# Kernel tuning notes

Hardware: AMD Instinct MI355X
Metric: run time of the kernel (lower is better)

## Reference

```python
import jax, jax.numpy as jnp
import numpy as np

H, W = 512, 512  # image_size from init_kwargs


def _render_single(xyz, color, opacity):
    """Faithful JAX version of GaussianRenderer._fallback_render (the path the
    module executes when the CUDA rasterizer is unavailable), vectorized.
    Point-splat each Gaussian to one pixel, depth-sort descending (back-to-front),
    alpha-composite: a_k = o_k * prod_{j<k}(1 - o_j); depth = z of front-most hit.
    xyz: (N,3)  color: (N,3)  opacity: (N,1)
    """
    N = xyz.shape[0]
    focal = (H + W) / 2.0
    z = xyz[:, 2]
    xf = xyz[:, 0] / (z + 1e-6) * focal + W / 2.0
    yf = xyz[:, 1] / (z + 1e-6) * focal + H / 2.0
    # torch .long() truncates toward zero
    xi = jnp.trunc(jnp.clip(xf, -1e9, 1e9)).astype(jnp.int32)
    yi = jnp.trunc(jnp.clip(yf, -1e9, 1e9)).astype(jnp.int32)
    valid = (xi >= 0) & (xi < W) & (yi >= 0) & (yi < H)
    pix = jnp.where(valid, yi * W + xi, H * W)  # dummy slot H*W for out-of-bounds
    # stable sort: primary pixel ascending, secondary z descending (back-to-front)
    order = jnp.lexsort((-z, pix))
    pix_s, z_s = pix[order], z[order]
    o_s = opacity[order, 0]
    c_s = color[order]
    valid_s = pix_s < H * W
    # per-pixel exclusive transmittance: alpha recurrence 1-A_k = (1-A_{k-1})(1-o_k)
    logt = jnp.log(jnp.clip(1.0 - o_s, 1e-12, None))
    cs = jnp.cumsum(logt)
    excl = cs - logt  # exclusive cumsum (global)
    start = jnp.concatenate([jnp.ones((1,), bool), pix_s[1:] != pix_s[:-1]])
    start_idx = jax.lax.cummax(jnp.where(start, jnp.arange(N), -1))
    T_prev = jnp.exp(excl - excl[start_idx])  # exclusive within pixel segment
    a = jnp.where(valid_s, o_s * T_prev, 0.0)
    img = jnp.zeros((H * W + 1, 3), xyz.dtype).at[pix_s].add(a[:, None] * c_s)
    # depth: last element written per pixel (front-most, smallest z in segment)
    end = jnp.concatenate([pix_s[1:] != pix_s[:-1], jnp.ones((1,), bool)])
    dpix = jnp.where(end & valid_s, pix_s, H * W)
    depth = jnp.zeros((H * W + 1,), xyz.dtype).at[dpix].set(z_s)
    render = img[: H * W].reshape(H, W, 3).transpose(2, 0, 1)  # (3,H,W)
    return render, depth[: H * W].reshape(1, H, W)


def setup_inputs() -> dict:
    key = jax.random.key(0)
    ks = jax.random.split(key, 5)
    B, N = 8, 262144
    return {
        "xyz": jax.random.normal(ks[0], (B, N, 3), jnp.float32),
        "scale": jax.random.normal(ks[1], (B, N, 3), jnp.float32),
        "rotation": jax.random.normal(ks[2], (B, N, 1), jnp.float32),
        "opacity": jax.random.uniform(ks[3], (B, N, 1), jnp.float32),
        "color": jax.random.uniform(ks[4], (B, N, 3), jnp.float32),
    }


def reference(xyz, scale, rotation, opacity, color):
    # scale/rotation are accepted (part of the gaussians dict) but unused by the
    # fallback renderer, matching the torch source.
    render, depth = jax.vmap(_render_single)(xyz, color, opacity)
    return render, depth
```

## Files before the change

### kernel.cpp

```cpp
#include <hip/hip_runtime.h>
#include <hip/hip_fp16.h>
#include <stdint.h>

#define W_ 512
#define H_ 512
#define HW_ (512 * 512)
#define RMAX 6
#define OVF_CAP 65536

__device__ __forceinline__ int project_pix(float x, float y, float z) {
    float zz = z + 1e-6f;
    float xf = x / zz * 512.0f + 256.0f;
    float yf = y / zz * 512.0f + 256.0f;
    xf = fminf(fmaxf(xf, -1e9f), 1e9f);
    yf = fminf(fmaxf(yf, -1e9f), 1e9f);
    int xi = (int)xf;
    int yi = (int)yf;
    if (xi >= 0 && xi < W_ && yi >= 0 && yi < H_) return yi * W_ + xi;
    return -1;
}

__device__ __forceinline__ float lo_h(unsigned int u) {
    return __half2float(__ushort_as_half((unsigned short)(u & 0xffffu)));
}
__device__ __forceinline__ float hi_h(unsigned int u) {
    return __half2float(__ushort_as_half((unsigned short)(u >> 16)));
}

__global__ void __launch_bounds__(256) k_init(uint4* __restrict__ p, int n4) {
    int i = blockIdx.x * blockDim.x + threadIdx.x;
    if (i < n4) p[i] = make_uint4(0u, 0u, 0u, 0u);
}

__global__ void __launch_bounds__(256) k_build(const float4* __restrict__ xyz4,
                                               const float4* __restrict__ op4,
                                               const float4* __restrict__ col4,
                                               unsigned int* __restrict__ cnt,
                                               uint4* __restrict__ slots,
                                               unsigned int* __restrict__ ovf_hdr,
                                               unsigned int* __restrict__ ovf_pix,
                                               uint4* __restrict__ ovf_rec,
                                               int N, int total4) {
    int t = blockIdx.x * blockDim.x + threadIdx.x;
    if (t >= total4) return;
    float4 v0 = xyz4[3 * (size_t)t + 0];
    float4 v1 = xyz4[3 * (size_t)t + 1];
    float4 v2 = xyz4[3 * (size_t)t + 2];
    float4 o4 = op4[t];
    float4 c0 = col4[3 * (size_t)t + 0];
    float4 c1 = col4[3 * (size_t)t + 1];
    float4 c2 = col4[3 * (size_t)t + 2];
    float xs[4] = {v0.x, v0.w, v1.z, v2.y};
    float ys[4] = {v0.y, v1.x, v1.w, v2.z};
    float zs[4] = {v0.z, v1.y, v2.x, v2.w};
    float os[4] = {o4.x, o4.y, o4.z, o4.w};
    float cr[4] = {c0.x, c0.w, c1.z, c2.y};
    float cg[4] = {c0.y, c1.x, c1.w, c2.z};
    float cb[4] = {c0.z, c1.y, c2.x, c2.w};
    int g0 = 4 * t;
    size_t pbase = (size_t)(g0 / N) * HW_;
#pragma unroll
    for (int j = 0; j < 4; ++j) {
        int pix = project_pix(xs[j], ys[j], zs[j]);
        if (pix >= 0) {
            size_t p = pbase + pix;
            unsigned int s = atomicAdd(&cnt[p], 1u);
            uint4 rec;
            rec.x = __float_as_uint(zs[j]);
            rec.y = (unsigned int)(g0 + j);
            rec.z = (unsigned int)__half_as_ushort(__float2half_rn(os[j])) |
                    ((unsigned int)__half_as_ushort(__float2half_rn(cr[j])) << 16);
            rec.w = (unsigned int)__half_as_ushort(__float2half_rn(cg[j])) |
                    ((unsigned int)__half_as_ushort(__float2half_rn(cb[j])) << 16);
            if (s < RMAX) {
                slots[p * RMAX + s] = rec;
            } else {
                unsigned int i = atomicAdd(ovf_hdr, 1u);
                if (i < OVF_CAP) { ovf_pix[i] = (unsigned int)p; ovf_rec[i] = rec; }
            }
        }
    }
}

__global__ void __launch_bounds__(256) k_composite(const unsigned int* __restrict__ cnt,
                                                   const uint4* __restrict__ slots,
                                                   const unsigned int* __restrict__ ovf_hdr,
                                                   const unsigned int* __restrict__ ovf_pix,
                                                   const uint4* __restrict__ ovf_rec,
                                                   float* __restrict__ out, int B) {
    int q = blockIdx.x * blockDim.x + threadIdx.x;
    int nb4 = B * (HW_ / 4);
    if (q >= nb4) return;
    int p0 = 4 * q;
    int b = p0 / HW_;
    int pl = p0 - b * HW_;

    uint4 c4 = ((const uint4*)cnt)[q];
    unsigned int ks[4] = {c4.x, c4.y, c4.z, c4.w};
    float r4[4], g4[4], b4[4], d4[4];

#pragma unroll
    for (int j = 0; j < 4; ++j) {
        int k = (int)ks[j];
        float r = 0.f, g2 = 0.f, bl = 0.f, depth = 0.f, T = 1.f;
        if (k > 0) {
            size_t sbase = (size_t)(p0 + j) * RMAX;
            if (k <= RMAX) {
                float z_[8];
                int   i_[8];
                unsigned int pa_[8], pb_[8];
#pragma unroll
                for (int t = 0; t < 8; ++t) {
                    if (t < RMAX && t < k) {
                        uint4 rec = slots[sbase + t];
                        z_[t] = __uint_as_float(rec.x);
                        i_[t] = (int)rec.y;
                        pa_[t] = rec.z;
                        pb_[t] = rec.w;
                    } else {
                        z_[t] = -__builtin_inff();
                        i_[t] = 0x7fffffff;
                        pa_[t] = 0u;
                        pb_[t] = 0u;
                    }
                }
#define CE(I, J)                                                                  \
                {                                                                 \
                    bool sw = (z_[J] > z_[I]) || (z_[J] == z_[I] && i_[J] < i_[I]); \
                    if (sw) {                                                     \
                        float tz = z_[I]; z_[I] = z_[J]; z_[J] = tz;              \
                        int ti = i_[I]; i_[I] = i_[J]; i_[J] = ti;                \
                        unsigned int ta = pa_[I]; pa_[I] = pa_[J]; pa_[J] = ta;   \
                        unsigned int tb = pb_[I]; pb_[I] = pb_[J]; pb_[J] = tb;   \
                    }                                                             \
                }
                CE(0,1) CE(2,3) CE(4,5) CE(6,7)
                CE(0,2) CE(1,3) CE(4,6) CE(5,7)
                CE(1,2) CE(5,6)
                CE(0,4) CE(1,5) CE(2,6) CE(3,7)
                CE(2,4) CE(3,5)
                CE(1,2) CE(3,4) CE(5,6)
#undef CE
#pragma unroll
                for (int t = 0; t < RMAX; ++t) {
                    if (t < k) {
                        float o  = lo_h(pa_[t]);
                        float rr = hi_h(pa_[t]);
                        float gg = lo_h(pb_[t]);
                        float bb = hi_h(pb_[t]);
                        float a = o * T;
                        r  += a * rr;
                        g2 += a * gg;
                        bl += a * bb;
                        T *= (1.0f - o);
                        depth = z_[t];
                    }
                }
            } else {
                unsigned int nov = ovf_hdr[0];
                if (nov > OVF_CAP) nov = OVF_CAP;
                unsigned int ptag = (unsigned int)(p0 + j);
                float prev_z = __builtin_inff();
                int prev_i = -1;
                for (int s = 0; s < k; ++s) {
                    float best_z = -__builtin_inff();
                    int best_i = 0x7fffffff;
                    unsigned int ba = 0u, bb2 = 0u;
                    for (int t2 = 0; t2 < RMAX; ++t2) {
                        uint4 rec = slots[sbase + t2];
                        float z = __uint_as_float(rec.x);
                        int   i = (int)rec.y;
                        bool after  = (z < prev_z) || (z == prev_z && i > prev_i);
                        bool better = (z > best_z) || (z == best_z && i < best_i);
                        if (after && better) { best_z = z; best_i = i; ba = rec.z; bb2 = rec.w; }
                    }
                    for (unsigned int t2 = 0; t2 < nov; ++t2) {
                        if (ovf_pix[t2] == ptag) {
                            uint4 rec = ovf_rec[t2];
                            float z = __uint_as_float(rec.x);
                            int   i = (int)rec.y;
                            bool after  = (z < prev_z) || (z == prev_z && i > prev_i);
                            bool better = (z > best_z) || (z == best_z && i < best_i);
                            if (after && better) { best_z = z; best_i = i; ba = rec.z; bb2 = rec.w; }
                        }
                    }
                    float o  = lo_h(ba);
                    float rr = hi_h(ba);
                    float gg = lo_h(bb2);
                    float bb = hi_h(bb2);
                    float a = o * T;
                    r  += a * rr;
                    g2 += a * gg;
                    bl += a * bb;
                    T *= (1.0f - o);
                    depth = best_z;
                    prev_z = best_z;
                    prev_i = best_i;
                }
            }
        }
        r4[j] = r; g4[j] = g2; b4[j] = bl; d4[j] = depth;
    }

    size_t HWs = (size_t)HW_;
    *(float4*)(out + ((size_t)b * 3 + 0) * HWs + pl) = make_float4(r4[0], r4[1], r4[2], r4[3]);
    *(float4*)(out + ((size_t)b * 3 + 1) * HWs + pl) = make_float4(g4[0], g4[1], g4[2], g4[3]);
    *(float4*)(out + ((size_t)b * 3 + 2) * HWs + pl) = make_float4(b4[0], b4[1], b4[2], b4[3]);
    *(float4*)(out + (size_t)B * 3 * HWs + (size_t)b * HWs + pl) =
        make_float4(d4[0], d4[1], d4[2], d4[3]);
}

extern "C" void kernel_launch(void* const* d_in, const int* in_sizes, int n_in,
                              void* d_out, int out_size, void* d_ws, size_t ws_size,
                              hipStream_t stream) {
    const float* xyz     = (const float*)d_in[0];
    const float* opacity = (const float*)d_in[3];
    const float* color   = (const float*)d_in[4];
    float* out = (float*)d_out;

    int B = out_size / (4 * HW_);
    int N = in_sizes[0] / (3 * B);
    int total = B * N;
    int nb = B * HW_;

    unsigned int* cnt     = (unsigned int*)d_ws;
    unsigned int* ovf_hdr = cnt + nb;
    unsigned int* ovf_pix = ovf_hdr + 1024;
    uint4*        ovf_rec = (uint4*)(ovf_pix + OVF_CAP);
    uint4*        slots   = ovf_rec + OVF_CAP;

    int blk = 256;
    int zw4 = (nb + 1024) / 4;
    k_init<<<(zw4 + blk - 1) / blk, blk, 0, stream>>>((uint4*)cnt, zw4);

    int total4 = total / 4;
    k_build<<<(total4 + blk - 1) / blk, blk, 0, stream>>>((const float4*)xyz,
                                                          (const float4*)opacity,
                                                          (const float4*)color,
                                                          cnt, slots, ovf_hdr, ovf_pix, ovf_rec,
                                                          N, total4);

    int nb4 = nb / 4;
    k_composite<<<(nb4 + blk - 1) / blk, blk, 0, stream>>>(cnt, slots, ovf_hdr, ovf_pix, ovf_rec,
                                                           out, B);
}
```

Baseline: 44.78 us.

## Pack per-pixel counters to 16 bits and compact occupied pixels in composite

Per-pixel counters shrink from 32-bit to 16-bit pairs, which halves counter init and read traffic. Opacity and colour are now gathered only for Gaussians that project in bounds, instead of always loading full float4s. The composite kernel zero-fills outputs with vector stores, builds a shared-memory queue of occupied pixels, and processes only those. This cuts divergence and slot reads for the many empty pixels. RMAX drops to 4 with a smaller sorting network, so more pixels spill to the slow linear-scan overflow path. It also adds scattered scalar output stores and a shared atomic per occupied pixel.

```diff
diff --git a/kernel.cpp b/kernel.cpp
--- a/kernel.cpp
+++ b/kernel.cpp
@@ -5,8 +5,10 @@
 #define W_ 512
 #define H_ 512
 #define HW_ (512 * 512)
-#define RMAX 6
+#define RMAX 4
 #define OVF_CAP 65536
+#define PXB 2048
+#define CTHR 256
 
 __device__ __forceinline__ int project_pix(float x, float y, float z) {
     float zz = z + 1e-6f;
@@ -33,8 +35,8 @@
 }
 
 __global__ void __launch_bounds__(256) k_build(const float4* __restrict__ xyz4,
-                                               const float4* __restrict__ op4,
-                                               const float4* __restrict__ col4,
+                                               const float* __restrict__ op,
+                                               const float* __restrict__ col,
                                                unsigned int* __restrict__ cnt,
                                                uint4* __restrict__ slots,
                                                unsigned int* __restrict__ ovf_hdr,
@@ -46,32 +48,31 @@
     float4 v0 = xyz4[3 * (size_t)t + 0];
     float4 v1 = xyz4[3 * (size_t)t + 1];
     float4 v2 = xyz4[3 * (size_t)t + 2];
-    float4 o4 = op4[t];
-    float4 c0 = col4[3 * (size_t)t + 0];
-    float4 c1 = col4[3 * (size_t)t + 1];
-    float4 c2 = col4[3 * (size_t)t + 2];
     float xs[4] = {v0.x, v0.w, v1.z, v2.y};
     float ys[4] = {v0.y, v1.x, v1.w, v2.z};
     float zs[4] = {v0.z, v1.y, v2.x, v2.w};
-    float os[4] = {o4.x, o4.y, o4.z, o4.w};
-    float cr[4] = {c0.x, c0.w, c1.z, c2.y};
-    float cg[4] = {c0.y, c1.x, c1.w, c2.z};
-    float cb[4] = {c0.z, c1.y, c2.x, c2.w};
     int g0 = 4 * t;
     size_t pbase = (size_t)(g0 / N) * HW_;
 #pragma unroll
     for (int j = 0; j < 4; ++j) {
         int pix = project_pix(xs[j], ys[j], zs[j]);
         if (pix >= 0) {
+            int g = g0 + j;
             size_t p = pbase + pix;
-            unsigned int s = atomicAdd(&cnt[p], 1u);
+            unsigned int sh = 16u * (unsigned int)(p & 1);
+            unsigned int old = atomicAdd(&cnt[p >> 1], 1u << sh);
+            unsigned int s = (old >> sh) & 0xffffu;
+            float o  = op[g];
+            float cr = col[3 * (size_t)g + 0];
+            float cg = col[3 * (size_t)g + 1];
+            float cb = col[3 * (size_t)g + 2];
             uint4 rec;
             rec.x = __float_as_uint(zs[j]);
-            rec.y = (unsigned int)(g0 + j);
-            rec.z = (unsigned int)__half_as_ushort(__float2half_rn(os[j])) |
-                    ((unsigned int)__half_as_ushort(__float2half_rn(cr[j])) << 16);
-            rec.w = (unsigned int)__half_as_ushort(__float2half_rn(cg[j])) |
-                    ((unsigned int)__half_as_ushort(__float2half_rn(cb[j])) << 16);
+            rec.y = (unsigned int)g;
+            rec.z = (unsigned int)__half_as_ushort(__float2half_rn(o)) |
+                    ((unsigned int)__half_as_ushort(__float2half_rn(cr)) << 16);
+            rec.w = (unsigned int)__half_as_ushort(__float2half_rn(cg)) |
+                    ((unsigned int)__half_as_ushort(__float2half_rn(cb)) << 16);
             if (s < RMAX) {
                 slots[p * RMAX + s] = rec;
             } else {
@@ -82,132 +83,151 @@
     }
 }
 
-__global__ void __launch_bounds__(256) k_composite(const unsigned int* __restrict__ cnt,
-                                                   const uint4* __restrict__ slots,
-                                                   const unsigned int* __restrict__ ovf_hdr,
-                                                   const unsigned int* __restrict__ ovf_pix,
-                                                   const uint4* __restrict__ ovf_rec,
-                                                   float* __restrict__ out, int B) {
-    int q = blockIdx.x * blockDim.x + threadIdx.x;
-    int nb4 = B * (HW_ / 4);
-    if (q >= nb4) return;
-    int p0 = 4 * q;
-    int b = p0 / HW_;
-    int pl = p0 - b * HW_;
-
-    uint4 c4 = ((const uint4*)cnt)[q];
-    unsigned int ks[4] = {c4.x, c4.y, c4.z, c4.w};
-    float r4[4], g4[4], b4[4], d4[4];
-
-#pragma unroll
-    for (int j = 0; j < 4; ++j) {
-        int k = (int)ks[j];
+__global__ void __launch_bounds__(CTHR) k_composite(const unsigned int* __restrict__ cnt,
+                                                    const uint4* __restrict__ slots,
+                                                    const unsigned int* __restrict__ ovf_hdr,
+                                                    const unsigned int* __restrict__ ovf_pix,
+                                                    const uint4* __restrict__ ovf_rec,
+                                                    float* __restrict__ out, int B) {
+    __shared__ unsigned int q[PXB];
+    __shared__ unsigned int qn;
+    int t = threadIdx.x;
+    if (t == 0) qn = 0u;
+    __syncthreads();
+
+    int pb0 = blockIdx.x * PXB;
+    int b = pb0 / HW_;
+    int pl0 = pb0 - b * HW_;
+    size_t HWs = (size_t)HW_;
+    float* oR = out + ((size_t)b * 3 + 0) * HWs;
+    float* oG = out + ((size_t)b * 3 + 1) * HWs;
+    float* oB = out + ((size_t)b * 3 + 2) * HWs;
+    float* oD = out + (size_t)B * 3 * HWs + (size_t)b * HWs;
+
+    uint4 cw = ((const uint4*)cnt)[(pb0 >> 3) + t];
+    unsigned int ws[4] = {cw.x, cw.y, cw.z, cw.w};
+
+    int pz = pl0 + t * 8;
+    float4 z4 = make_float4(0.f, 0.f, 0.f, 0.f);
+    *(float4*)(oR + pz) = z4; *(float4*)(oR + pz + 4) = z4;
+    *(float4*)(oG + pz) = z4; *(float4*)(oG + pz + 4) = z4;
+    *(float4*)(oB + pz) = z4; *(float4*)(oB + pz + 4) = z4;
+    *(float4*)(oD + pz) = z4; *(float4*)(oD + pz + 4) = z4;
+
+#pragma unroll
+    for (int j = 0; j < 8; ++j) {
+        unsigned int k = (ws[j >> 1] >> (16 * (j & 1))) & 0xffffu;
+        if (k) {
+            unsigned int i = atomicAdd(&qn, 1u);
+            q[i] = (k << 16) | (unsigned int)(t * 8 + j);
+        }
+    }
+    __syncthreads();
+
+    unsigned int n = qn;
+    for (unsigned int i = t; i < n; i += CTHR) {
+        unsigned int e = q[i];
+        int k = (int)(e >> 16);
+        int id = (int)(e & 0xffffu);
+        size_t p = (size_t)pb0 + id;
+        size_t sbase = p * RMAX;
         float r = 0.f, g2 = 0.f, bl = 0.f, depth = 0.f, T = 1.f;
-        if (k > 0) {
-            size_t sbase = (size_t)(p0 + j) * RMAX;
-            if (k <= RMAX) {
-                float z_[8];
-                int   i_[8];
-                unsigned int pa_[8], pb_[8];
-#pragma unroll
-                for (int t = 0; t < 8; ++t) {
-                    if (t < RMAX && t < k) {
-                        uint4 rec = slots[sbase + t];
-                        z_[t] = __uint_as_float(rec.x);
-                        i_[t] = (int)rec.y;
-                        pa_[t] = rec.z;
-                        pb_[t] = rec.w;
-                    } else {
-                        z_[t] = -__builtin_inff();
-                        i_[t] = 0x7fffffff;
-                        pa_[t] = 0u;
-                        pb_[t] = 0u;
-                    }
-                }
-#define CE(I, J)                                                                  \
-                {                                                                 \
-                    bool sw = (z_[J] > z_[I]) || (z_[J] == z_[I] && i_[J] < i_[I]); \
-                    if (sw) {                                                     \
-                        float tz = z_[I]; z_[I] = z_[J]; z_[J] = tz;              \
-                        int ti = i_[I]; i_[I] = i_[J]; i_[J] = ti;                \
-                        unsigned int ta = pa_[I]; pa_[I] = pa_[J]; pa_[J] = ta;   \
-                        unsigned int tb = pb_[I]; pb_[I] = pb_[J]; pb_[J] = tb;   \
-                    }                                                             \
-                }
-                CE(0,1) CE(2,3) CE(4,5) CE(6,7)
-                CE(0,2) CE(1,3) CE(4,6) CE(5,7)
-                CE(1,2) CE(5,6)
-                CE(0,4) CE(1,5) CE(2,6) CE(3,7)
-                CE(2,4) CE(3,5)
-                CE(1,2) CE(3,4) CE(5,6)
+
+        if (k <= RMAX) {
+            float z_[RMAX];
+            int   i_[RMAX];
+            unsigned int pa_[RMAX], pb_[RMAX];
+#pragma unroll
+            for (int s = 0; s < RMAX; ++s) {
+                if (s < k) {
+                    uint4 rec = slots[sbase + s];
+                    z_[s] = __uint_as_float(rec.x);
+                    i_[s] = (int)rec.y;
+                    pa_[s] = rec.z;
+                    pb_[s] = rec.w;
+                } else {
+                    z_[s] = -__builtin_inff();
+                    i_[s] = 0x7fffffff;
+                    pa_[s] = 0u;
+                    pb_[s] = 0u;
+                }
+            }
+#define CE(I, J)                                                              \
+            {                                                                 \
+                bool sw = (z_[J] > z_[I]) || (z_[J] == z_[I] && i_[J] < i_[I]); \
+                if (sw) {                                                     \
+                    float tz = z_[I]; z_[I] = z_[J]; z_[J] = tz;              \
+                    int ti = i_[I]; i_[I] = i_[J]; i_[J] = ti;                \
+                    unsigned int ta = pa_[I]; pa_[I] = pa_[J]; pa_[J] = ta;   \
+                    unsigned int tb = pb_[I]; pb_[I] = pb_[J]; pb_[J] = tb;   \
+                }                                                             \
+            }
+            CE(0,1) CE(2,3) CE(0,2) CE(1,3) CE(1,2)
 #undef CE
 #pragma unroll
-                for (int t = 0; t < RMAX; ++t) {
-                    if (t < k) {
-                        float o  = lo_h(pa_[t]);
-                        float rr = hi_h(pa_[t]);
-                        float gg = lo_h(pb_[t]);
-                        float bb = hi_h(pb_[t]);
-                        float a = o * T;
-                        r  += a * rr;
-                        g2 += a * gg;
-                        bl += a * bb;
-                        T *= (1.0f - o);
-                        depth = z_[t];
-                    }
-                }
-            } else {
-                unsigned int nov = ovf_hdr[0];
-                if (nov > OVF_CAP) nov = OVF_CAP;
-                unsigned int ptag = (unsigned int)(p0 + j);
-                float prev_z = __builtin_inff();
-                int prev_i = -1;
-                for (int s = 0; s < k; ++s) {
-                    float best_z = -__builtin_inff();
-                    int best_i = 0x7fffffff;
-                    unsigned int ba = 0u, bb2 = 0u;
-                    for (int t2 = 0; t2 < RMAX; ++t2) {
-                        uint4 rec = slots[sbase + t2];
-                        float z = __uint_as_float(rec.x);
-                        int   i = (int)rec.y;
-                        bool after  = (z < prev_z) || (z == prev_z && i > prev_i);
-                        bool better = (z > best_z) || (z == best_z && i < best_i);
-                        if (after && better) { best_z = z; best_i = i; ba = rec.z; bb2 = rec.w; }
-                    }
-                    for (unsigned int t2 = 0; t2 < nov; ++t2) {
-                        if (ovf_pix[t2] == ptag) {
-                            uint4 rec = ovf_rec[t2];
-                            float z = __uint_as_float(rec.x);
-                            int   i = (int)rec.y;
-                            bool after  = (z < prev_z) || (z == prev_z && i > prev_i);
-                            bool better = (z > best_z) || (z == best_z && i < best_i);
-                            if (after && better) { best_z = z; best_i = i; ba = rec.z; bb2 = rec.w; }
-                        }
-                    }
-                    float o  = lo_h(ba);
-                    float rr = hi_h(ba);
-                    float gg = lo_h(bb2);
-                    float bb = hi_h(bb2);
+            for (int s = 0; s < RMAX; ++s) {
+                if (s < k) {
+                    float o  = lo_h(pa_[s]);
+                    float rr = hi_h(pa_[s]);
+                    float gg = lo_h(pb_[s]);
+                    float bb = hi_h(pb_[s]);
                     float a = o * T;
                     r  += a * rr;
                     g2 += a * gg;
                     bl += a * bb;
                     T *= (1.0f - o);
-                    depth = best_z;
-                    prev_z = best_z;
-                    prev_i = best_i;
-                }
+                    depth = z_[s];
+                }
+            }
+        } else {
+            unsigned int nov = ovf_hdr[0];
+            if (nov > OVF_CAP) nov = OVF_CAP;
+            unsigned int ptag = (unsigned int)p;
+            float prev_z = __builtin_inff();
+            int prev_i = -1;
+            for (int s = 0; s < k; ++s) {
+                float best_z = -__builtin_inff();
+                int best_i = 0x7fffffff;
+                unsigned int ba = 0u, bb2 = 0u;
+                for (int t2 = 0; t2 < RMAX; ++t2) {
+                    uint4 rec = slots[sbase + t2];
+                    float z = __uint_as_float(rec.x);
+                    int   i2 = (int)rec.y;
+                    bool after  = (z < prev_z) || (z == prev_z && i2 > prev_i);
+                    bool better = (z > best_z) || (z == best_z && i2 < best_i);
+                    if (after && better) { best_z = z; best_i = i2; ba = rec.z; bb2 = rec.w; }
+                }
+                for (unsigned int t2 = 0; t2 < nov; ++t2) {
+                    if (ovf_pix[t2] == ptag) {
+                        uint4 rec = ovf_rec[t2];
+                        float z = __uint_as_float(rec.x);
+                        int   i2 = (int)rec.y;
+                        bool after  = (z < prev_z) || (z == prev_z && i2 > prev_i);
+                        bool better = (z > best_z) || (z == best_z && i2 < best_i);
+                        if (after && better) { best_z = z; best_i = i2; ba = rec.z; bb2 = rec.w; }
+                    }
+                }
+                float o  = lo_h(ba);
+                float rr = hi_h(ba);
+                float gg = lo_h(bb2);
+                float bb = hi_h(bb2);
+                float a = o * T;
+                r  += a * rr;
+                g2 += a * gg;
+                bl += a * bb;
+                T *= (1.0f - o);
+                depth = best_z;
+                prev_z = best_z;
+                prev_i = best_i;
             }
         }
-        r4[j] = r; g4[j] = g2; b4[j] = bl; d4[j] = depth;
+
+        int pl = pl0 + id;
+        oR[pl] = r;
+        oG[pl] = g2;
+        oB[pl] = bl;
+        oD[pl] = depth;
     }
-
-    size_t HWs = (size_t)HW_;
-    *(float4*)(out + ((size_t)b * 3 + 0) * HWs + pl) = make_float4(r4[0], r4[1], r4[2], r4[3]);
-    *(float4*)(out + ((size_t)b * 3 + 1) * HWs + pl) = make_float4(g4[0], g4[1], g4[2], g4[3]);
-    *(float4*)(out + ((size_t)b * 3 + 2) * HWs + pl) = make_float4(b4[0], b4[1], b4[2], b4[3]);
-    *(float4*)(out + (size_t)B * 3 * HWs + (size_t)b * HWs + pl) =
-        make_float4(d4[0], d4[1], d4[2], d4[3]);
 }
 
 extern "C" void kernel_launch(void* const* d_in, const int* in_sizes, int n_in,
@@ -224,23 +244,22 @@
     int nb = B * HW_;
 
     unsigned int* cnt     = (unsigned int*)d_ws;
-    unsigned int* ovf_hdr = cnt + nb;
+    unsigned int* ovf_hdr = cnt + nb / 2;
     unsigned int* ovf_pix = ovf_hdr + 1024;
     uint4*        ovf_rec = (uint4*)(ovf_pix + OVF_CAP);
     uint4*        slots   = ovf_rec + OVF_CAP;
 
     int blk = 256;
-    int zw4 = (nb + 1024) / 4;
-    k_init<<<(zw4 + blk - 1) / blk, blk, 0, stream>>>((uint4*)cnt, zw4);
+    int zwords = nb / 2 + 1024;
+    int z4 = zwords / 4;
+    k_init<<<(z4 + blk - 1) / blk, blk, 0, stream>>>((uint4*)cnt, z4);
 
     int total4 = total / 4;
     k_build<<<(total4 + blk - 1) / blk, blk, 0, stream>>>((const float4*)xyz,
-                                                          (const float4*)opacity,
-                                                          (const float4*)color,
+                                                          opacity, color,
                                                           cnt, slots, ovf_hdr, ovf_pix, ovf_rec,
                                                           N, total4);
 
-    int nb4 = nb / 4;
-    k_composite<<<(nb4 + blk - 1) / blk, blk, 0, stream>>>(cnt, slots, ovf_hdr, ovf_pix, ovf_rec,
-                                                           out, B);
-}
+    int nblk = nb / PXB;
+    k_composite<<<nblk, CTHR, 0, stream>>>(cnt, slots, ovf_hdr, ovf_pix, ovf_rec, out, B);
+}
```

Result: slower. 45.72 us (+2.1%).
